# Performance work log

Measured on AMD Instinct MI355X. Metric: run time of the kernel, lower is better.

The kernel has to match this reference:

```python
import jax, jax.numpy as jnp
import numpy as np

HEADS = 8
DIM_HEAD = 64
DIM = 128
TOPK = (8, 8, 8)  # depth, height, width


def chan_ln(x, g, b):
    # channel layernorm over axis=1 (biased variance), eps added to std
    mean = jnp.mean(x, axis=1, keepdims=True)
    var = jnp.var(x, axis=1, keepdims=True)
    return g * (x - mean) / (jnp.sqrt(var) + 1e-6) + b


def l2norm(x):
    # F.normalize(dim=1): divide by max(||x||_2, eps)
    n = jnp.sqrt(jnp.sum(x * x, axis=1, keepdims=True))
    return x / jnp.maximum(n, 1e-12)


def _forward(query_source, context, w_q, w_kv, w_out,
             ctx_gamma, ctx_beta, qs_gamma, qs_beta, out_gamma, out_beta, gamma):
    b, c, Dq, Hq, Wq = query_source.shape
    Dc, Hc, Wc = context.shape[2:]
    kd, kh, kw = TOPK

    ctx = chan_ln(context, ctx_gamma, ctx_beta)
    qs = chan_ln(query_source, qs_gamma, qs_beta)

    # 1x1x1 convs == channel matmuls
    kv = jnp.einsum('bcdhw,oc->bodhw', ctx, w_kv)   # (b, 2*inner, D, H, W)
    k, v = jnp.split(kv, 2, axis=1)
    q = jnp.einsum('bcdhw,oc->bodhw', qs, w_q)      # (b, inner, D, H, W)

    def fold(t):  # (b, h*c, D,H,W) -> (b*h, c, D,H,W)
        return t.reshape(b * HEADS, DIM_HEAD, *t.shape[2:])

    q, k, v = fold(q), fold(k), fold(v)
    q, k = l2norm(q), l2norm(k)

    q_probe = jnp.sum(q, axis=(2, 3, 4))            # (bh, c)
    k_abs = jnp.abs(k)

    if kd < Dc:
        score = jnp.einsum('bc,bcd->bd', q_probe, jnp.sum(k_abs, axis=(3, 4)))
        idx = jax.lax.top_k(score, kd)[1][:, None, :, None, None]
        k = jnp.take_along_axis(k, idx, axis=2)
        v = jnp.take_along_axis(v, idx, axis=2)
    if kh < Hc:
        score = jnp.einsum('bc,bch->bh', q_probe, jnp.sum(k_abs, axis=(2, 4)))
        idx = jax.lax.top_k(score, kh)[1][:, None, None, :, None]
        k = jnp.take_along_axis(k, idx, axis=3)
        v = jnp.take_along_axis(v, idx, axis=3)
    if kw < Wc:
        score = jnp.einsum('bc,bcw->bw', q_probe, jnp.sum(k_abs, axis=(2, 3)))
        idx = jax.lax.top_k(score, kw)[1][:, None, None, None, :]
        k = jnp.take_along_axis(k, idx, axis=4)
        v = jnp.take_along_axis(v, idx, axis=4)

    def flat(t):  # (bh, c, d, h, w) -> (bh, d*h*w, c)
        return t.reshape(t.shape[0], t.shape[1], -1).transpose(0, 2, 1)

    qf, kf, vf = flat(q), flat(k), flat(v)
    sim = jnp.einsum('bic,bjc->bij', qf, kf)        # (bh, Nq, Nkv)
    attn = jax.nn.softmax(sim, axis=-1)
    out = jnp.einsum('bij,bjc->bic', attn, vf)      # (bh, Nq, c)

    out = out.reshape(b, HEADS, Dq, Hq, Wq, DIM_HEAD)
    out = out.transpose(0, 1, 5, 2, 3, 4).reshape(b, HEADS * DIM_HEAD, Dq, Hq, Wq)
    out = jnp.einsum('bcdhw,oc->bodhw', out, w_out)
    out = chan_ln(out, out_gamma, out_beta)
    return gamma * out + query_source


def setup_inputs() -> dict:
    key = jax.random.key(0)
    ks = jax.random.split(key, 6)
    b, c, D, H, W = 2, DIM, 16, 32, 32
    inner = HEADS * DIM_HEAD
    ones = jnp.ones((1, c, 1, 1, 1), jnp.float32)
    zeros = jnp.zeros((1, c, 1, 1, 1), jnp.float32)
    return {
        'query_source': jax.random.normal(ks[0], (b, c, D, H, W), jnp.float32),
        'context': jax.random.normal(ks[1], (b, c, D, H, W), jnp.float32),
        'w_q': jax.random.normal(ks[2], (inner, c), jnp.float32) / np.sqrt(c).astype(np.float32),
        'w_kv': jax.random.normal(ks[3], (2 * inner, c), jnp.float32) / np.sqrt(c).astype(np.float32),
        'w_out': jax.random.normal(ks[4], (c, inner), jnp.float32) / np.sqrt(inner).astype(np.float32),
        'ctx_gamma': ones, 'ctx_beta': zeros,
        'qs_gamma': ones, 'qs_beta': zeros,
        'out_gamma': ones, 'out_beta': zeros,
        'gamma': jnp.full((1,), 0.5, jnp.float32),
    }


def reference(query_source, context, w_q, w_kv, w_out,
              ctx_gamma, ctx_beta, qs_gamma, qs_beta, out_gamma, out_beta, gamma):
    return _forward(query_source, context, w_q, w_kv, w_out,
                    ctx_gamma, ctx_beta, qs_gamma, qs_beta, out_gamma, out_beta, gamma)
```

## Files before the change

### kernel.cpp

```cpp
#include <hip/hip_runtime.h>
#include <hip/hip_bf16.h>

#define S_SP 16384
#define NKV 512

typedef short short8 __attribute__((ext_vector_type(8)));
typedef float v4f   __attribute__((ext_vector_type(4)));

__device__ __forceinline__ unsigned short f2bf(float x){
  union { float f; unsigned u; } v; v.f = x;
  unsigned r = v.u + 0x7FFFu + ((v.u >> 16) & 1u);
  return (unsigned short)(r >> 16);
}
__device__ __forceinline__ float bf2f(unsigned short h){
  union { unsigned u; float f; } v; v.u = ((unsigned)h) << 16; return v.f;
}

#if defined(__has_builtin)
#if __has_builtin(__builtin_amdgcn_cvt_pk_bf16_f32)
#define HAVE_PKBF 1
#endif
#endif

__device__ __forceinline__ unsigned pk2(float a, float b){
#ifdef HAVE_PKBF
  typedef __bf16 bf16x2 __attribute__((ext_vector_type(2)));
  union { bf16x2 v; unsigned u; } r;
  r.v = __builtin_amdgcn_cvt_pk_bf16_f32(a, b);
  return r.u;
#else
  return (unsigned)f2bf(a) | ((unsigned)f2bf(b) << 16);
#endif
}

__global__ __launch_bounds__(256) void k_stats(const float* __restrict__ ctx,
                                               const float* __restrict__ qs,
                                               float* __restrict__ MEAN,
                                               float* __restrict__ INV){
  __shared__ float r1[4][64];
  __shared__ float r2[4][64];
  int bx = blockIdx.x;
  int tt = bx >> 9; int b = (bx >> 8) & 1; int sc = bx & 255;
  int t = threadIdx.x;
  int sv = t & 63, cg = t >> 6;
  int s = sc*64 + sv;
  const float* src = (tt ? qs : ctx) + ((size_t)b*128 + cg*32)*S_SP + s;
  float sum = 0.f, ss = 0.f;
  #pragma unroll 8
  for (int c = 0; c < 32; c++){
    float v = src[(size_t)c*S_SP];
    sum += v; ss += v*v;
  }
  r1[cg][sv] = sum; r2[cg][sv] = ss;
  __syncthreads();
  if (t < 64){
    float sm = r1[0][t]+r1[1][t]+r1[2][t]+r1[3][t];
    float sq = r2[0][t]+r2[1][t]+r2[2][t]+r2[3][t];
    float mean = sm * 0.0078125f;
    float var  = fmaxf(sq * 0.0078125f - mean*mean, 0.f);
    int o = tt*2*S_SP + b*S_SP + sc*64 + t;
    MEAN[o] = mean;
    INV[o]  = 1.f/(sqrtf(var) + 1e-6f);
  }
}

template<int ISK>
__global__ __launch_bounds__(256) void k_projT(
    const float* __restrict__ src, const float* __restrict__ wmat,
    const float* __restrict__ gam, const float* __restrict__ bet,
    const float* __restrict__ MEAN, const float* __restrict__ INV,
    unsigned short* __restrict__ QBF, float* __restrict__ QP,
    float* __restrict__ SCORE){
  __shared__ __align__(16) float xlds[32*256];
  __shared__ __align__(16) float wlds[32*128];
  __shared__ float nbuf[4][256];
  __shared__ float ibuf[2][256];
  __shared__ float qpl[128];
  __shared__ float SCP[4][44];
  int bx = blockIdx.x;
  int og = bx & 3, stile = (bx>>2)&63, b = bx>>8;
  int s0 = stile*256;
  int t = threadIdx.x;
  int w = t>>6, lane = t&63;
  int ow0 = w*32;
  int tt = ISK ? 0 : 1;
  const float* Mn = MEAN + tt*32768 + b*16384 + s0;
  const float* Iv = INV  + tt*32768 + b*16384 + s0;
  const float* WB = wmat + (size_t)og*128*128;
  if (ISK){ if (t < 128) qpl[t] = QP[(b*8 + og*2)*64 + t]; }
  int col = lane*4;
  v4f mv = *(const v4f*)(Mn + col);
  v4f vv = *(const v4f*)(Iv + col);
  v4f acc[32];
  #pragma unroll
  for (int i=0;i<32;i++) acc[i] = (v4f){0.f,0.f,0.f,0.f};
  for (int kc=0;kc<4;kc++){
    __syncthreads();
    #pragma unroll
    for (int i=0;i<8;i++){
      int kk = i*4 + w;
      int cgl = kc*32 + kk;
      v4f xv = *(const v4f*)(src + ((size_t)(b*128+cgl))*S_SP + s0 + col);
      float gg = gam[cgl], bb = bet[cgl];
      v4f r;
      #pragma unroll
      for (int j=0;j<4;j++) r[j] = gg*(xv[j]-mv[j])*vv[j] + bb;
      *(v4f*)&xlds[kk*256 + col] = r;
    }
    {
      int oc = t>>1, ks0 = (t&1)*16;
      const float* wr = WB + (size_t)oc*128 + kc*32 + ks0;
      v4f w0 = *(const v4f*)wr, w1 = *(const v4f*)(wr+4);
      v4f w2 = *(const v4f*)(wr+8), w3 = *(const v4f*)(wr+12);
      #pragma unroll
      for (int i=0;i<4;i++){
        wlds[(ks0+i   )*128+oc]=w0[i];
        wlds[(ks0+i+4 )*128+oc]=w1[i];
        wlds[(ks0+i+8 )*128+oc]=w2[i];
        wlds[(ks0+i+12)*128+oc]=w3[i];
      }
    }
    __syncthreads();
    #pragma unroll 2
    for (int kk=0;kk<32;kk++){
      v4f xv = *(const v4f*)&xlds[kk*256 + col];
      #pragma unroll
      for (int o8=0;o8<8;o8++){
        v4f w4 = *(const v4f*)&wlds[kk*128 + ow0 + o8*4];
        acc[o8*4+0] += xv*w4[0];
        acc[o8*4+1] += xv*w4[1];
        acc[o8*4+2] += xv*w4[2];
        acc[o8*4+3] += xv*w4[3];
      }
    }
  }
  v4f ss = {0.f,0.f,0.f,0.f};
  #pragma unroll
  for (int o=0;o<32;o++) ss += acc[o]*acc[o];
  *(v4f*)&nbuf[w][col] = ss;
  __syncthreads();
  if (t < 256){
    float a0 = nbuf[0][t]+nbuf[1][t];
    float a1 = nbuf[2][t]+nbuf[3][t];
    ibuf[0][t] = 1.f/fmaxf(sqrtf(a0),1e-12f);
    ibuf[1][t] = 1.f/fmaxf(sqrtf(a1),1e-12f);
  }
  __syncthreads();
  int hl = w>>1;
  v4f iv4 = *(const v4f*)&ibuf[hl][col];
  int head = og*2 + hl, bh = b*8 + head;
  if (!ISK){
    #pragma unroll
    for (int o=0;o<32;o++) acc[o] *= iv4;
    #pragma unroll
    for (int j=0;j<4;j++){
      int s = s0 + col + j;
      unsigned short* dst = QBF + ((size_t)bh*S_SP + s)*64 + (w&1)*32;
      #pragma unroll
      for (int v=0;v<4;v++){
        uint4 pk;
        pk.x = pk2(acc[v*8+0][j], acc[v*8+1][j]);
        pk.y = pk2(acc[v*8+2][j], acc[v*8+3][j]);
        pk.z = pk2(acc[v*8+4][j], acc[v*8+5][j]);
        pk.w = pk2(acc[v*8+6][j], acc[v*8+7][j]);
        *(uint4*)(dst + v*8) = pk;
      }
    }
    float mine = 0.f;
    #pragma unroll
    for (int o=0;o<32;o++){
      float v = acc[o][0]+acc[o][1]+acc[o][2]+acc[o][3];
      v += __shfl_xor(v,1,64); v += __shfl_xor(v,2,64); v += __shfl_xor(v,4,64);
      v += __shfl_xor(v,8,64); v += __shfl_xor(v,16,64); v += __shfl_xor(v,32,64);
      if (lane == o) mine = v;
    }
    if (lane < 32) atomicAdd(QP + bh*64 + (w&1)*32 + lane, mine);
  } else {
    v4f tj = {0.f,0.f,0.f,0.f};
    #pragma unroll
    for (int o=0;o<32;o++){
      float qw = qpl[ow0+o];
      v4f av;
      #pragma unroll
      for (int j=0;j<4;j++) av[j] = fabsf(acc[o][j]);
      tj += av*qw;
    }
    tj *= iv4;
    v4f twv = tj;
    #pragma unroll
    for (int m=8;m<=32;m<<=1){
      v4f o2;
      #pragma unroll
      for (int j=0;j<4;j++) o2[j] = __shfl_xor(twv[j], m, 64);
      twv += o2;
    }
    float th = tj[0]+tj[1]+tj[2]+tj[3];
    th += __shfl_xor(th,1,64); th += __shfl_xor(th,2,64); th += __shfl_xor(th,4,64);
    float td = twv[0]+twv[1]+twv[2]+twv[3];
    td += __shfl_xor(td,1,64); td += __shfl_xor(td,2,64); td += __shfl_xor(td,4,64);
    if (lane == 0) SCP[w][0] = td;
    if ((lane&7) == 0) SCP[w][1 + (lane>>3)] = th;
    if (lane < 8){
      #pragma unroll
      for (int j=0;j<4;j++) SCP[w][9 + lane*4 + j] = twv[j];
    }
    __syncthreads();
    if (t < 82){
      int hl2 = t/41, slot = t - hl2*41;
      float v = SCP[hl2*2][slot] + SCP[hl2*2+1][slot];
      int bh2 = b*8 + og*2 + hl2;
      int off;
      if (slot == 0) off = stile>>2;
      else if (slot < 9) off = 16 + (stile&3)*8 + (slot-1);
      else off = 48 + (slot-9);
      atomicAdd(SCORE + bh2*80 + off, v);
    }
  }
}

__global__ __launch_bounds__(64) void k_topk(const float* __restrict__ SCORE,
                                             int* __restrict__ IDX){
  int bh = blockIdx.x;
  if (threadIdx.x != 0) return;
  float sc[80];
  for (int i=0;i<80;i++) sc[i] = SCORE[bh*80+i];
  for (int a=0;a<3;a++){
    int n = a ? 32 : 16;
    int off = (a==0) ? 0 : (a==1 ? 16 : 48);
    for (int it=0; it<8; it++){
      int bi = 0; float bv = -3.4e38f;
      for (int i=0;i<n;i++){ float v = sc[off+i]; if (v > bv){ bv=v; bi=i; } }
      IDX[bh*24 + a*8 + it] = bi;
      sc[off+bi] = -3.4e38f;
    }
  }
}

__global__ __launch_bounds__(256) void k_gather(const float* __restrict__ ctx,
    const float* __restrict__ wkv, const float* __restrict__ ctx_g,
    const float* __restrict__ ctx_b, const float* __restrict__ MEAN,
    const float* __restrict__ INV, const int* __restrict__ IDX,
    unsigned short* __restrict__ KG, unsigned short* __restrict__ VGT){
  __shared__ float wlds[64*129];
  __shared__ float xln[32*128];
  __shared__ int sidx[24];
  int bx = blockIdx.x;
  int bh = bx >> 5, jc = (bx >> 1) & 15, type = bx & 1;
  int head = bh & 7, b = bh >> 3;
  int t = threadIdx.x;
  if (t < 24) sidx[t] = IDX[bh*24 + t];
  {
    int oc = t>>2, ks = (t&3)*32;
    const float* wr = wkv + ((size_t)(type*512 + head*64 + oc))*128 + ks;
    #pragma unroll 8
    for (int i=0;i<32;i++) wlds[oc*129 + ks + i] = wr[i];
  }
  __syncthreads();
  {
    int jl = t>>3, seg = (t&7)*16;
    int jj = jc*32 + jl;
    int dsel = sidx[jj>>6], hsel = sidx[8 + ((jj>>3)&7)], wsel = sidx[16 + (jj&7)];
    int sj = dsel*1024 + hsel*32 + wsel;
    float mn = MEAN[b*S_SP + sj];
    float iv = INV[b*S_SP + sj];
    #pragma unroll
    for (int i=0;i<16;i++){
      int cc = seg + i;
      float raw = ctx[((size_t)(b*128 + cc))*S_SP + sj];
      xln[jl*128 + cc] = ctx_g[cc]*(raw - mn)*iv + ctx_b[cc];
    }
  }
  __syncthreads();
  int c = t & 63, jg = t >> 6;
  float accv[8] = {};
  #pragma unroll 4
  for (int k=0;k<128;k++){
    float wv = wlds[c*129 + k];
    #pragma unroll
    for (int m=0;m<8;m++) accv[m] += wv * xln[(jg + 4*m)*128 + k];
  }
  #pragma unroll
  for (int m=0;m<8;m++){
    int jj = jc*32 + jg + 4*m;
    float a = accv[m];
    if (type == 0){
      float sq = a*a;
      #pragma unroll
      for (int mm=32; mm; mm>>=1) sq += __shfl_xor(sq, mm, 64);
      float rn = 1.f/fmaxf(sqrtf(sq), 1e-12f);
      KG[((size_t)bh*NKV + jj)*64 + c] = f2bf(a*rn);
    } else {
      VGT[((size_t)bh*64 + c)*NKV + jj] = f2bf(a);
    }
  }
}

__global__ __launch_bounds__(256) void k_attn(const unsigned short* __restrict__ QBF,
    const unsigned short* __restrict__ KG, const unsigned short* __restrict__ VGT,
    unsigned short* __restrict__ AOUT){
  __shared__ __align__(16) unsigned short kst[128*72];
  __shared__ __align__(16) unsigned short vst[64*136];
  __shared__ __align__(16) unsigned short pst[4][64*40];
  int bx = blockIdx.x;
  int bh = bx >> 6, qb = bx & 63;
  int t = threadIdx.x;
  int wvi = t >> 6, lane = t & 63;
  int quad = lane >> 4, l15 = lane & 15;
  int q0 = qb*256 + wvi*64;
  const unsigned short* kgb = KG + (size_t)bh*NKV*64;
  const unsigned short* vgb = VGT + (size_t)bh*64*NKV;
  short8 bq[4][2];
  #pragma unroll
  for (int qt=0; qt<4; qt++){
    const unsigned short* qp_ = QBF + ((size_t)bh*S_SP + q0 + qt*16 + l15)*64 + quad*8;
    union { uint4 u; short8 s; } u0, u1;
    u0.u = *(const uint4*)(qp_);
    u1.u = *(const uint4*)(qp_ + 32);
    bq[qt][0] = u0.s; bq[qt][1] = u1.s;
  }
  v4f oacc[4][4];
  #pragma unroll
  for (int i=0;i<4;i++)
    #pragma unroll
    for (int j=0;j<4;j++) oacc[i][j] = (v4f){0.f,0.f,0.f,0.f};
  float lsum[4] = {0.f,0.f,0.f,0.f};
  unsigned short* pw = pst[wvi];
  for (int ch=0; ch<4; ch++){
    __syncthreads();
    {
      int jl = t>>1, hf = (t&1)*32;
      const unsigned short* sp = kgb + (size_t)(ch*128 + jl)*64 + hf;
      unsigned short* dp = kst + jl*72 + hf;
      #pragma unroll
      for (int i=0;i<4;i++) *(uint4*)(dp + i*8) = *(const uint4*)(sp + i*8);
    }
    {
      int cc = t>>2, js = (t&3)*32;
      const unsigned short* sp = vgb + (size_t)cc*NKV + ch*128 + js;
      unsigned short* dp = vst + cc*136 + js;
      #pragma unroll
      for (int i=0;i<4;i++) *(uint4*)(dp + i*8) = *(const uint4*)(sp + i*8);
    }
    __syncthreads();
    #pragma unroll
    for (int sub=0; sub<4; sub++){
      v4f s[2][4];
      #pragma unroll
      for (int j2=0; j2<2; j2++){
        int jt = sub*2 + j2;
        const unsigned short* kr = kst + (jt*16 + l15)*72 + quad*8;
        union { uint4 u; short8 s; } a0, a1;
        a0.u = *(const uint4*)(kr);
        a1.u = *(const uint4*)(kr + 32);
        #pragma unroll
        for (int qt=0; qt<4; qt++){
          v4f z = {0.f,0.f,0.f,0.f};
          z = __builtin_amdgcn_mfma_f32_16x16x32_bf16(a0.s, bq[qt][0], z, 0, 0, 0);
          z = __builtin_amdgcn_mfma_f32_16x16x32_bf16(a1.s, bq[qt][1], z, 0, 0, 0);
          s[j2][qt] = z;
        }
      }
      #pragma unroll
      for (int j2=0; j2<2; j2++){
        #pragma unroll
        for (int qt=0; qt<4; qt++){
          v4f p;
          #pragma unroll
          for (int r=0;r<4;r++) p[r] = __expf(s[j2][qt][r] - 1.0f);
          lsum[qt] += p[0]+p[1]+p[2]+p[3];
          uint2 wv;
          wv.x = pk2(p[0], p[1]);
          wv.y = pk2(p[2], p[3]);
          *(uint2*)&pw[(qt*16 + l15)*40 + j2*16 + quad*4] = wv;
        }
      }
      short8 bp[4];
      #pragma unroll
      for (int qt=0; qt<4; qt++){
        union { uint4 u; short8 s; } ub;
        ub.u = *(const uint4*)&pw[(qt*16 + l15)*40 + quad*8];
        bp[qt] = ub.s;
      }
      #pragma unroll
      for (int ct=0; ct<4; ct++){
        union { uint4 u; short8 s; } av;
        av.u = *(const uint4*)&vst[(ct*16 + l15)*136 + sub*32 + quad*8];
        #pragma unroll
        for (int qt=0; qt<4; qt++)
          oacc[ct][qt] = __builtin_amdgcn_mfma_f32_16x16x32_bf16(av.s, bp[qt], oacc[ct][qt], 0, 0, 0);
      }
    }
  }
  float rl[4];
  #pragma unroll
  for (int qt=0; qt<4; qt++){
    float l = lsum[qt];
    l += __shfl_xor(l, 16, 64);
    l += __shfl_xor(l, 32, 64);
    rl[qt] = 1.f/l;
  }
  #pragma unroll
  for (int qt=0; qt<4; qt++){
    #pragma unroll
    for (int ct=0; ct<4; ct++){
      v4f o = oacc[ct][qt];
      uint2 wv;
      wv.x = pk2(o[0]*rl[qt], o[1]*rl[qt]);
      wv.y = pk2(o[2]*rl[qt], o[3]*rl[qt]);
      *(uint2*)(AOUT + ((size_t)bh*S_SP + q0 + qt*16 + l15)*64 + ct*16 + quad*4) = wv;
    }
  }
}

__global__ __launch_bounds__(256) void k_out(const unsigned short* __restrict__ AOUT,
    const float* __restrict__ wout, const float* __restrict__ out_g,
    const float* __restrict__ out_b, const float* __restrict__ gamma,
    const float* __restrict__ qsrc, float* __restrict__ OUT){
  __shared__ __align__(16) unsigned short wl[128*40];
  __shared__ float lnp[4][2][64];
  __shared__ float mbuf[64], sbuf[64], ogl[128], obl[128];
  int bx = blockIdx.x; int b = bx>>8; int stile = bx&255; int s0 = stile*64;
  int t = threadIdx.x; int w = t>>6; int lane = t&63;
  int q = lane>>4; int l15 = lane&15;
  if (t < 128){ ogl[t] = out_g[t]; obl[t] = out_b[t]; }
  v4f acc[2][4];
  #pragma unroll
  for (int i=0;i<2;i++)
    #pragma unroll
    for (int j=0;j<4;j++) acc[i][j] = (v4f){0.f,0.f,0.f,0.f};
  for (int kt=0; kt<16; kt++){
    __syncthreads();
    {
      int c = t>>1, kb = (t&1)*16;
      const float* wr = wout + (size_t)c*512 + kt*32 + kb;
      v4f a0 = *(const v4f*)wr, a1 = *(const v4f*)(wr+4);
      v4f a2 = *(const v4f*)(wr+8), a3 = *(const v4f*)(wr+12);
      uint4 u0, u1;
      u0.x = pk2(a0[0], a0[1]); u0.y = pk2(a0[2], a0[3]);
      u0.z = pk2(a1[0], a1[1]); u0.w = pk2(a1[2], a1[3]);
      u1.x = pk2(a2[0], a2[1]); u1.y = pk2(a2[2], a2[3]);
      u1.z = pk2(a3[0], a3[1]); u1.w = pk2(a3[2], a3[3]);
      *(uint4*)&wl[c*40+kb]   = u0;
      *(uint4*)&wl[c*40+kb+8] = u1;
    }
    __syncthreads();
    short8 af[2];
    #pragma unroll
    for (int mt=0;mt<2;mt++){
      union { uint4 u; short8 s; } ua;
      ua.u = *(const uint4*)&wl[(w*32+mt*16+l15)*40 + q*8];
      af[mt] = ua.s;
    }
    int head = kt>>1; int cc0 = (kt&1)*32 + q*8;
    const unsigned short* bp = AOUT + ((size_t)((b*8+head)*S_SP + s0 + l15))*64 + cc0;
    #pragma unroll
    for (int nt=0;nt<4;nt++){
      union { uint4 u; short8 s; } ub;
      ub.u = *(const uint4*)(bp + (size_t)nt*16*64);
      #pragma unroll
      for (int mt=0;mt<2;mt++)
        acc[mt][nt] = __builtin_amdgcn_mfma_f32_16x16x32_bf16(af[mt], ub.s, acc[mt][nt], 0, 0, 0);
    }
  }
  #pragma unroll
  for (int nt=0;nt<4;nt++){
    float p1 = 0.f, p2 = 0.f;
    #pragma unroll
    for (int mt=0;mt<2;mt++)
      #pragma unroll
      for (int r=0;r<4;r++){ float v = acc[mt][nt][r]; p1 += v; p2 += v*v; }
    p1 += __shfl_xor(p1,16,64); p1 += __shfl_xor(p1,32,64);
    p2 += __shfl_xor(p2,16,64); p2 += __shfl_xor(p2,32,64);
    if (q == 0){ lnp[w][0][nt*16+l15] = p1; lnp[w][1][nt*16+l15] = p2; }
  }
  __syncthreads();
  if (t < 64){
    float m = (lnp[0][0][t]+lnp[1][0][t]+lnp[2][0][t]+lnp[3][0][t]) * 0.0078125f;
    float qq = (lnp[0][1][t]+lnp[1][1][t]+lnp[2][1][t]+lnp[3][1][t]) * 0.0078125f;
    float var = fmaxf(qq - m*m, 0.f);
    mbuf[t] = m;
    sbuf[t] = 1.f/(sqrtf(var) + 1e-6f);
  }
  __syncthreads();
  float gs = gamma[0];
  #pragma unroll
  for (int nt=0;nt<4;nt++){
    int sl = nt*16 + l15;
    float mm = mbuf[sl], ssc = sbuf[sl];
    #pragma unroll
    for (int mt=0;mt<2;mt++){
      #pragma unroll
      for (int r=0;r<4;r++){
        int c = w*32 + mt*16 + q*4 + r;
        size_t adr = ((size_t)(b*128+c))*S_SP + s0 + sl;
        float yn = (acc[mt][nt][r]-mm)*ssc;
        OUT[adr] = gs*(ogl[c]*yn + obl[c]) + qsrc[adr];
      }
    }
  }
}

extern "C" void kernel_launch(void* const* d_in, const int* in_sizes, int n_in,
                              void* d_out, int out_size, void* d_ws, size_t ws_size,
                              hipStream_t stream){
  const float* qsrc  = (const float*)d_in[0];
  const float* ctx   = (const float*)d_in[1];
  const float* wq    = (const float*)d_in[2];
  const float* wkv   = (const float*)d_in[3];
  const float* wout  = (const float*)d_in[4];
  const float* ctx_g = (const float*)d_in[5];
  const float* ctx_b = (const float*)d_in[6];
  const float* qs_g  = (const float*)d_in[7];
  const float* qs_b  = (const float*)d_in[8];
  const float* out_g = (const float*)d_in[9];
  const float* out_b = (const float*)d_in[10];
  const float* gamma = (const float*)d_in[11];
  float* OUT = (float*)d_out;
  char* ws = (char*)d_ws;
  float* QP    = (float*)(ws);
  float* SCORE = (float*)(ws + 4096);
  float* MEAN  = (float*)(ws + 16384);
  float* INV   = (float*)(ws + 278528);
  int*   IDX   = (int*)(ws + 540672);
  unsigned short* QBF  = (unsigned short*)(ws + 544768);
  unsigned short* KG   = (unsigned short*)(ws + 34099200);
  unsigned short* VGT  = (unsigned short*)(ws + 35147776);
  unsigned short* AOUT = (unsigned short*)(ws + 36196352);

  hipMemsetAsync(ws, 0, 9216, stream);
  k_stats<<<1024, 256, 0, stream>>>(ctx, qsrc, MEAN, INV);
  k_projT<0><<<512, 256, 0, stream>>>(qsrc, wq, qs_g, qs_b, MEAN, INV, QBF, QP, SCORE);
  k_projT<1><<<512, 256, 0, stream>>>(ctx, wkv, ctx_g, ctx_b, MEAN, INV, QBF, QP, SCORE);
  k_topk<<<16, 64, 0, stream>>>(SCORE, IDX);
  k_gather<<<512, 256, 0, stream>>>(ctx, wkv, ctx_g, ctx_b, MEAN, INV, IDX, KG, VGT);
  k_attn<<<1024, 256, 0, stream>>>(QBF, KG, VGT, AOUT);
  k_out<<<512, 256, 0, stream>>>(AOUT, wout, out_g, out_b, gamma, qsrc, OUT);
}
```

Measured before the change: 341.0 us.

## Restructure attention with async LDS double-buffering and register-resident P, pre-convert w_out

The attention kernel now uses 512-thread blocks and loads K/V tiles into shared memory via global_load_lds DMA, double-buffering K across chunks. It feeds the exp'd scores straight from registers into 16x16x16 MFMAs against V, so the P round-trip through shared memory goes away. The output projection now reads a bf16 copy of w_out made once by a new conversion kernel, dropping the per-block conversion and its barriers. The risks are extra register pressure, narrower scalar AOUT stores, and correctness depending on hand-tuned waitcnt barriers.

```diff
diff --git a/kernel.cpp b/kernel.cpp
--- a/kernel.cpp
+++ b/kernel.cpp
@@ -5,6 +5,7 @@
 #define NKV 512
 
 typedef short short8 __attribute__((ext_vector_type(8)));
+typedef short short4_t __attribute__((ext_vector_type(4)));
 typedef float v4f   __attribute__((ext_vector_type(4)));
 
 __device__ __forceinline__ unsigned short f2bf(float x){
@@ -31,6 +32,34 @@
 #else
   return (unsigned)f2bf(a) | ((unsigned)f2bf(b) << 16);
 #endif
+}
+
+__device__ __forceinline__ v4f mfma16(short4_t a, short4_t b, v4f c){
+#if __has_builtin(__builtin_amdgcn_mfma_f32_16x16x16bf16_1k)
+  return __builtin_amdgcn_mfma_f32_16x16x16bf16_1k(a, b, c, 0, 0, 0);
+#else
+  asm volatile("s_nop 1\n\tv_mfma_f32_16x16x16_bf16 %0, %1, %2, %0"
+               : "+v"(c) : "v"(a), "v"(b));
+  return c;
+#endif
+}
+
+__device__ __forceinline__ void dma16(const void* g, void* l){
+  __builtin_amdgcn_global_load_lds((const __attribute__((address_space(1))) unsigned int*)g,
+                                   (__attribute__((address_space(3))) unsigned int*)l, 16, 0, 0);
+}
+__device__ __forceinline__ void bar_lgkm(){ asm volatile("s_waitcnt lgkmcnt(0)\n\ts_barrier" ::: "memory"); }
+__device__ __forceinline__ void bar_vm2(){ asm volatile("s_waitcnt vmcnt(2)\n\ts_barrier" ::: "memory"); }
+__device__ __forceinline__ void bar_vm0(){ asm volatile("s_waitcnt vmcnt(0)\n\ts_barrier" ::: "memory"); }
+
+__global__ __launch_bounds__(256) void k_wcvt(const float* __restrict__ w,
+                                              unsigned short* __restrict__ o){
+  int i = (blockIdx.x*256 + threadIdx.x)*8;
+  v4f a = *(const v4f*)(w+i), b = *(const v4f*)(w+i+4);
+  uint4 u;
+  u.x = pk2(a[0],a[1]); u.y = pk2(a[2],a[3]);
+  u.z = pk2(b[0],b[1]); u.w = pk2(b[2],b[3]);
+  *(uint4*)(o+i) = u;
 }
 
 __global__ __launch_bounds__(256) void k_stats(const float* __restrict__ ctx,
@@ -295,20 +324,26 @@
   }
 }
 
-__global__ __launch_bounds__(256) void k_attn(const unsigned short* __restrict__ QBF,
+__global__ __launch_bounds__(512, 4) void k_attn(const unsigned short* __restrict__ QBF,
     const unsigned short* __restrict__ KG, const unsigned short* __restrict__ VGT,
     unsigned short* __restrict__ AOUT){
-  __shared__ __align__(16) unsigned short kst[128*72];
-  __shared__ __align__(16) unsigned short vst[64*136];
-  __shared__ __align__(16) unsigned short pst[4][64*40];
+  __shared__ __align__(16) unsigned short kst0[8224];
+  __shared__ __align__(16) unsigned short kst1[8224];
+  __shared__ __align__(16) unsigned short vst[8432];
   int bx = blockIdx.x;
-  int bh = bx >> 6, qb = bx & 63;
+  int bh = bx >> 5, qb = bx & 31;
   int t = threadIdx.x;
-  int wvi = t >> 6, lane = t & 63;
+  int wv = t >> 6, lane = t & 63;
   int quad = lane >> 4, l15 = lane & 15;
-  int q0 = qb*256 + wvi*64;
+  int q0 = qb*512 + wv*64;
   const unsigned short* kgb = KG + (size_t)bh*NKV*64;
   const unsigned short* vgb = VGT + (size_t)bh*64*NKV;
+  const unsigned short* ksrcA = kgb + ((size_t)(wv*8 + (lane>>3))*64 + (lane&7)*8);
+  const unsigned short* vsrcA = vgb + ((size_t)(wv*4 + (lane>>4))*512 + (lane&15)*8);
+  int kdoffA = wv*512 + (wv&1)*32;
+  unsigned short* vdstA = vst + wv*528;
+  int koff = (l15>>3)*544 + (l15&7)*64 + quad*8;
+  int voff = (l15>>2)*528 + (l15&3)*128 + quad*4;
   short8 bq[4][2];
   #pragma unroll
   for (int qt=0; qt<4; qt++){
@@ -324,99 +359,73 @@
     #pragma unroll
     for (int j=0;j<4;j++) oacc[i][j] = (v4f){0.f,0.f,0.f,0.f};
   float lsum[4] = {0.f,0.f,0.f,0.f};
-  unsigned short* pw = pst[wvi];
+  dma16(ksrcA, kst0 + kdoffA);
+  dma16(ksrcA + 4096, kst0 + kdoffA + 4096);
   for (int ch=0; ch<4; ch++){
-    __syncthreads();
-    {
-      int jl = t>>1, hf = (t&1)*32;
-      const unsigned short* sp = kgb + (size_t)(ch*128 + jl)*64 + hf;
-      unsigned short* dp = kst + jl*72 + hf;
-      #pragma unroll
-      for (int i=0;i<4;i++) *(uint4*)(dp + i*8) = *(const uint4*)(sp + i*8);
-    }
-    {
-      int cc = t>>2, js = (t&3)*32;
-      const unsigned short* sp = vgb + (size_t)cc*NKV + ch*128 + js;
-      unsigned short* dp = vst + cc*136 + js;
-      #pragma unroll
-      for (int i=0;i<4;i++) *(uint4*)(dp + i*8) = *(const uint4*)(sp + i*8);
-    }
-    __syncthreads();
-    #pragma unroll
-    for (int sub=0; sub<4; sub++){
-      v4f s[2][4];
-      #pragma unroll
-      for (int j2=0; j2<2; j2++){
-        int jt = sub*2 + j2;
-        const unsigned short* kr = kst + (jt*16 + l15)*72 + quad*8;
-        union { uint4 u; short8 s; } a0, a1;
-        a0.u = *(const uint4*)(kr);
-        a1.u = *(const uint4*)(kr + 32);
+    unsigned short* kb = (ch&1) ? kst1 : kst0;
+    bar_lgkm();
+    dma16(vsrcA + ch*128, vdstA);
+    dma16(vsrcA + ch*128 + 16384, vdstA + 4224);
+    if (ch < 3){
+      unsigned short* kn = (ch&1) ? kst0 : kst1;
+      dma16(ksrcA + (ch+1)*8192, kn + kdoffA);
+      dma16(ksrcA + (ch+1)*8192 + 4096, kn + kdoffA + 4096);
+      bar_vm2();
+    } else {
+      bar_vm0();
+    }
+    #pragma unroll 2
+    for (int jt=0; jt<8; jt++){
+      const unsigned short* kr = kb + jt*1024 + koff;
+      union { uint4 u; short8 s; } a0, a1;
+      a0.u = *(const uint4*)(kr);
+      a1.u = *(const uint4*)(kr + 32);
+      short4_t bV[4];
+      #pragma unroll
+      for (int ct=0; ct<4; ct++){
+        union { uint2 u2; short4_t s; } vvv;
+        vvv.u2 = *(const uint2*)(vst + ct*2112 + voff + jt*16);
+        bV[ct] = vvv.s;
+      }
+      #pragma unroll
+      for (int qt=0; qt<4; qt++){
+        v4f z = {0.f,0.f,0.f,0.f};
+        z = __builtin_amdgcn_mfma_f32_16x16x32_bf16(a0.s, bq[qt][0], z, 0, 0, 0);
+        z = __builtin_amdgcn_mfma_f32_16x16x32_bf16(a1.s, bq[qt][1], z, 0, 0, 0);
+        v4f p;
         #pragma unroll
-        for (int qt=0; qt<4; qt++){
-          v4f z = {0.f,0.f,0.f,0.f};
-          z = __builtin_amdgcn_mfma_f32_16x16x32_bf16(a0.s, bq[qt][0], z, 0, 0, 0);
-          z = __builtin_amdgcn_mfma_f32_16x16x32_bf16(a1.s, bq[qt][1], z, 0, 0, 0);
-          s[j2][qt] = z;
-        }
+        for (int r=0;r<4;r++) p[r] = __expf(z[r] - 1.0f);
+        lsum[qt] += (p[0]+p[1]) + (p[2]+p[3]);
+        union { unsigned u[2]; short4_t s; } pa;
+        pa.u[0] = pk2(p[0], p[1]);
+        pa.u[1] = pk2(p[2], p[3]);
+        #pragma unroll
+        for (int ct=0; ct<4; ct++)
+          oacc[qt][ct] = mfma16(pa.s, bV[ct], oacc[qt][ct]);
       }
-      #pragma unroll
-      for (int j2=0; j2<2; j2++){
-        #pragma unroll
-        for (int qt=0; qt<4; qt++){
-          v4f p;
-          #pragma unroll
-          for (int r=0;r<4;r++) p[r] = __expf(s[j2][qt][r] - 1.0f);
-          lsum[qt] += p[0]+p[1]+p[2]+p[3];
-          uint2 wv;
-          wv.x = pk2(p[0], p[1]);
-          wv.y = pk2(p[2], p[3]);
-          *(uint2*)&pw[(qt*16 + l15)*40 + j2*16 + quad*4] = wv;
-        }
-      }
-      short8 bp[4];
-      #pragma unroll
-      for (int qt=0; qt<4; qt++){
-        union { uint4 u; short8 s; } ub;
-        ub.u = *(const uint4*)&pw[(qt*16 + l15)*40 + quad*8];
-        bp[qt] = ub.s;
-      }
-      #pragma unroll
-      for (int ct=0; ct<4; ct++){
-        union { uint4 u; short8 s; } av;
-        av.u = *(const uint4*)&vst[(ct*16 + l15)*136 + sub*32 + quad*8];
-        #pragma unroll
-        for (int qt=0; qt<4; qt++)
-          oacc[ct][qt] = __builtin_amdgcn_mfma_f32_16x16x32_bf16(av.s, bp[qt], oacc[ct][qt], 0, 0, 0);
-      }
-    }
-  }
-  float rl[4];
+    }
+  }
   #pragma unroll
   for (int qt=0; qt<4; qt++){
     float l = lsum[qt];
     l += __shfl_xor(l, 16, 64);
     l += __shfl_xor(l, 32, 64);
-    rl[qt] = 1.f/l;
-  }
-  #pragma unroll
-  for (int qt=0; qt<4; qt++){
-    #pragma unroll
-    for (int ct=0; ct<4; ct++){
-      v4f o = oacc[ct][qt];
-      uint2 wv;
-      wv.x = pk2(o[0]*rl[qt], o[1]*rl[qt]);
-      wv.y = pk2(o[2]*rl[qt], o[3]*rl[qt]);
-      *(uint2*)(AOUT + ((size_t)bh*S_SP + q0 + qt*16 + l15)*64 + ct*16 + quad*4) = wv;
+    float rl = 1.f / l;
+    #pragma unroll
+    for (int r=0; r<4; r++){
+      float rr = __shfl(rl, quad*4 + r, 64);
+      size_t base = ((size_t)bh*S_SP + q0 + qt*16 + quad*4 + r)*64 + l15;
+      #pragma unroll
+      for (int ct=0; ct<4; ct++)
+        AOUT[base + ct*16] = f2bf(oacc[qt][ct][r]*rr);
     }
   }
 }
 
 __global__ __launch_bounds__(256) void k_out(const unsigned short* __restrict__ AOUT,
-    const float* __restrict__ wout, const float* __restrict__ out_g,
+    const unsigned short* __restrict__ WBF, const float* __restrict__ out_g,
     const float* __restrict__ out_b, const float* __restrict__ gamma,
     const float* __restrict__ qsrc, float* __restrict__ OUT){
-  __shared__ __align__(16) unsigned short wl[128*40];
   __shared__ float lnp[4][2][64];
   __shared__ float mbuf[64], sbuf[64], ogl[128], obl[128];
   int bx = blockIdx.x; int b = bx>>8; int stile = bx&255; int s0 = stile*64;
@@ -428,38 +437,20 @@
   for (int i=0;i<2;i++)
     #pragma unroll
     for (int j=0;j<4;j++) acc[i][j] = (v4f){0.f,0.f,0.f,0.f};
+  #pragma unroll 4
   for (int kt=0; kt<16; kt++){
-    __syncthreads();
-    {
-      int c = t>>1, kb = (t&1)*16;
-      const float* wr = wout + (size_t)c*512 + kt*32 + kb;
-      v4f a0 = *(const v4f*)wr, a1 = *(const v4f*)(wr+4);
-      v4f a2 = *(const v4f*)(wr+8), a3 = *(const v4f*)(wr+12);
-      uint4 u0, u1;
-      u0.x = pk2(a0[0], a0[1]); u0.y = pk2(a0[2], a0[3]);
-      u0.z = pk2(a1[0], a1[1]); u0.w = pk2(a1[2], a1[3]);
-      u1.x = pk2(a2[0], a2[1]); u1.y = pk2(a2[2], a2[3]);
-      u1.z = pk2(a3[0], a3[1]); u1.w = pk2(a3[2], a3[3]);
-      *(uint4*)&wl[c*40+kb]   = u0;
-      *(uint4*)&wl[c*40+kb+8] = u1;
-    }
-    __syncthreads();
-    short8 af[2];
-    #pragma unroll
-    for (int mt=0;mt<2;mt++){
-      union { uint4 u; short8 s; } ua;
-      ua.u = *(const uint4*)&wl[(w*32+mt*16+l15)*40 + q*8];
-      af[mt] = ua.s;
-    }
+    union { uint4 u; short8 s; } af0, af1;
+    const unsigned short* wr = WBF + (size_t)(w*32 + l15)*512 + kt*32 + q*8;
+    af0.u = *(const uint4*)(wr);
+    af1.u = *(const uint4*)(wr + 16*512);
     int head = kt>>1; int cc0 = (kt&1)*32 + q*8;
     const unsigned short* bp = AOUT + ((size_t)((b*8+head)*S_SP + s0 + l15))*64 + cc0;
     #pragma unroll
     for (int nt=0;nt<4;nt++){
       union { uint4 u; short8 s; } ub;
       ub.u = *(const uint4*)(bp + (size_t)nt*16*64);
-      #pragma unroll
-      for (int mt=0;mt<2;mt++)
-        acc[mt][nt] = __builtin_amdgcn_mfma_f32_16x16x32_bf16(af[mt], ub.s, acc[mt][nt], 0, 0, 0);
+      acc[0][nt] = __builtin_amdgcn_mfma_f32_16x16x32_bf16(af0.s, ub.s, acc[0][nt], 0, 0, 0);
+      acc[1][nt] = __builtin_amdgcn_mfma_f32_16x16x32_bf16(af1.s, ub.s, acc[1][nt], 0, 0, 0);
     }
   }
   #pragma unroll
@@ -526,13 +517,15 @@
   unsigned short* KG   = (unsigned short*)(ws + 34099200);
   unsigned short* VGT  = (unsigned short*)(ws + 35147776);
   unsigned short* AOUT = (unsigned short*)(ws + 36196352);
+  unsigned short* WBF  = (unsigned short*)(ws + 69750784);
 
   hipMemsetAsync(ws, 0, 9216, stream);
+  k_wcvt<<<32, 256, 0, stream>>>(wout, WBF);
   k_stats<<<1024, 256, 0, stream>>>(ctx, qsrc, MEAN, INV);
   k_projT<0><<<512, 256, 0, stream>>>(qsrc, wq, qs_g, qs_b, MEAN, INV, QBF, QP, SCORE);
   k_projT<1><<<512, 256, 0, stream>>>(ctx, wkv, ctx_g, ctx_b, MEAN, INV, QBF, QP, SCORE);
   k_topk<<<16, 64, 0, stream>>>(SCORE, IDX);
   k_gather<<<512, 256, 0, stream>>>(ctx, wkv, ctx_g, ctx_b, MEAN, INV, IDX, KG, VGT);
-  k_attn<<<1024, 256, 0, stream>>>(QBF, KG, VGT, AOUT);
-  k_out<<<512, 256, 0, stream>>>(AOUT, wout, out_g, out_b, gamma, qsrc, OUT);
-}
+  k_attn<<<512, 512, 0, stream>>>(QBF, KG, VGT, AOUT);
+  k_out<<<512, 256, 0, stream>>>(AOUT, WBF, out_g, out_b, gamma, qsrc, OUT);
+}
```

Result: slower. 450.7 us (+32.2%).
